# Performance work log

Hardware: AMD Instinct MI355X
Metric: run time of the kernel (lower is better)

Reference implementation:

```python
import jax, jax.numpy as jnp
import numpy as np

N_W, N_E, N_UP, N_DN = 4096, 32, 16, 16
D, N_LAYERS, K_DET = 64, 3, 16
BOX = 6.0


def _ln(x, g, b, eps=1e-5):
    mu = x.mean(-1, keepdims=True)
    v = ((x - mu) ** 2).mean(-1, keepdims=True)
    return (x - mu) / jnp.sqrt(v + eps) * g + b


def setup_inputs() -> dict:
    key = jax.random.key(0)
    ks = jax.random.split(key, 24)
    f32 = jnp.float32

    def w(k, shape, s=0.1):
        return (jax.random.normal(k, shape) * s).astype(f32)

    cell = (BOX * jnp.eye(3)).astype(f32)
    twist = w(ks[0], (3,), 0.3)
    r_electrons = (jax.random.uniform(ks[1], (N_W, N_E, 3)) * BOX).astype(f32)
    inp = dict(
        r_electrons=r_electrons, cell=cell, twist=twist,
        W_e=w(ks[2], (3, D)), b_e=w(ks[3], (D,), 0.05),
        W_pw=w(ks[4], (6, D)), b_pw=w(ks[5], (D,), 0.05),
        W1=w(ks[6], (N_LAYERS, 3 * D, D)), b1=w(ks[7], (N_LAYERS, D), 0.05),
        W2=w(ks[8], (N_LAYERS, D, D)), b2=w(ks[9], (N_LAYERS, D), 0.05),
        ln_w=jnp.ones((N_LAYERS, D), f32), ln_b=jnp.zeros((N_LAYERS, D), f32),
        W_up=w(ks[10], (D, K_DET * N_UP)), b_up=w(ks[11], (K_DET * N_UP,), 0.05),
        W_dn=w(ks[12], (D, K_DET * N_DN)), b_dn=w(ks[13], (K_DET * N_DN,), 0.05),
        det_weights=jnp.zeros((K_DET,), f32),
        Wj1=w(ks[14], (1, 32)), bj1=w(ks[15], (32,), 0.05),
        Wj2=w(ks[16], (32, 32)), bj2=w(ks[17], (32,), 0.05),
        Wj3=w(ks[18], (32, 1)), bj3=w(ks[19], (1,), 0.05),
        jastrow_scale=jnp.asarray(0.1, f32),
    )
    return inp


def reference(r_electrons, cell, twist, W_e, b_e, W_pw, b_pw, W1, b1, W2, b2,
              ln_w, ln_b, W_up, b_up, W_dn, b_dn, det_weights,
              Wj1, bj1, Wj2, bj2, Wj3, bj3, jastrow_scale):
    L_inv = jnp.linalg.inv(cell)
    # wrap to cell via fractional coords
    s = r_electrons @ L_inv.T
    r = (s - jnp.floor(s)) @ cell  # [Nw, Ne, 3]
    # plane-wave features on wrapped positions
    s2 = r @ L_inv.T
    two_pi = 2.0 * jnp.pi
    pw = jnp.concatenate([jnp.sin(two_pi * s2), jnp.cos(two_pi * s2)], axis=-1)
    h = r @ W_e + b_e + pw @ W_pw + b_pw  # [Nw, Ne, D]
    # mean-field interaction layers
    for l in range(W1.shape[0]):
        hm = jnp.broadcast_to(h.mean(axis=1, keepdims=True), h.shape)
        x = jnp.concatenate([h, hm, h * hm], axis=-1)  # [Nw, Ne, 3D]
        delta = jax.nn.silu(x @ W1[l] + b1[l]) @ W2[l] + b2[l]
        h = _ln(h + delta, ln_w[l], ln_b[l])
    # minimum-image pairwise distances
    d = r[:, :, None, :] - r[:, None, :, :]  # [Nw, Ne, Ne, 3]
    sij = d @ L_inv.T
    vec = (sij - jnp.round(sij)) @ cell
    r_ij = jnp.linalg.norm(vec, axis=-1)  # [Nw, Ne, Ne]
    iu, ju = np.triu_indices(r.shape[1], 1)
    rp = r_ij[:, iu, ju][..., None]  # [Nw, P, 1]
    j = jax.nn.silu(rp @ Wj1 + bj1)
    j = jax.nn.silu(j @ Wj2 + bj2)
    j = (j @ Wj3 + bj3)[..., 0]
    jastrow = jastrow_scale * j.sum(axis=1)  # [Nw]
    # multi-determinant combine (vectorized over K via signed logsumexp)
    K = det_weights.shape[0]
    n_up = W_up.shape[1] // K
    n_dn = W_dn.shape[1] // K
    orb_up = h[:, :n_up] @ W_up + b_up  # [Nw, n_up, K*n_up]
    phi_up = jnp.moveaxis(orb_up.reshape(-1, n_up, K, n_up), 2, 1)  # [Nw,K,n_up,n_up]
    su, lu = jnp.linalg.slogdet(phi_up)
    orb_dn = h[:, n_up:] @ W_dn + b_dn
    phi_dn = jnp.moveaxis(orb_dn.reshape(-1, n_dn, K, n_dn), 2, 1)
    sd, ld = jnp.linalg.slogdet(phi_dn)
    logs = lu + ld + jnp.log(jax.nn.softmax(det_weights) + 1e-10)[None, :]  # [Nw,K]
    signs = su * sd
    m = jnp.max(logs, axis=1, keepdims=True)
    ssum = jnp.sum(signs * jnp.exp(logs - m), axis=1)
    log_psi = jastrow + m[:, 0] + jnp.log(jnp.abs(ssum) + 1e-30)
    sign_psi = jnp.sign(ssum)
    return log_psi, sign_psi
```

## Files before the change

kernel.cpp:

```cpp
#include <hip/hip_runtime.h>

#define N_WALK 4096
#define N_EL   32
#define DIM    64
#define HPAD   66
#define NLAY   3
#define KDET   16
#define NPAIR  496
#define TWO_PI_D 6.283185307179586476925286766559
#define JTAB_N    8192
#define JTAB_RMAX 5.25f

using f64x4 = __attribute__((ext_vector_type(4))) double;

#define MFMA64(A, B, C) __builtin_amdgcn_mfma_f64_16x16x4f64((A), (B), (C), 0, 0, 0)

__device__ __forceinline__ double exp_d(double x) {
  const double LOG2E  = 1.4426950408889634074;
  const double LN2_HI = 6.93147180369123816490e-01;
  const double LN2_LO = 1.90821492927058770002e-10;
  const double nf = rint(x * LOG2E);
  double r = fma(-nf, LN2_HI, x);
  r = fma(-nf, LN2_LO, r);
  double p = 1.0/3628800.0;
  p = fma(p, r, 1.0/362880.0);
  p = fma(p, r, 1.0/40320.0);
  p = fma(p, r, 1.0/5040.0);
  p = fma(p, r, 1.0/720.0);
  p = fma(p, r, 1.0/120.0);
  p = fma(p, r, 1.0/24.0);
  p = fma(p, r, 1.0/6.0);
  p = fma(p, r, 0.5);
  p = fma(p, r, 1.0);
  p = fma(p, r, 1.0);
  const long long bits = ((long long)((int)nf + 1023)) << 52;
  return p * __longlong_as_double(bits);
}

__device__ __forceinline__ double silu_d(double x) {
  const double d = 1.0 + exp_d(-x);
  const double q0 = (double)(1.0f / (float)d);
  double q = q0 * (2.0 - d * q0);
  q = q * (2.0 - d * q);
  return x * q;
}
__device__ __forceinline__ float silu_q(float x) { return x / (1.0f + __expf(-x)); }

__device__ __forceinline__ void sincos_2pi(double u, double* s, double* c) {
  const double q = rint(u * 4.0);
  const double z = fma(q, -0.25, u);
  const double th = z * TWO_PI_D;
  const double t2 = th * th;
  double ps = -1.0/39916800.0;
  ps = fma(ps, t2, 1.0/362880.0);
  ps = fma(ps, t2, -1.0/5040.0);
  ps = fma(ps, t2, 1.0/120.0);
  ps = fma(ps, t2, -1.0/6.0);
  ps = fma(ps, t2, 1.0);
  const double sn = th * ps;
  double pc = 1.0/479001600.0;
  pc = fma(pc, t2, -1.0/3628800.0);
  pc = fma(pc, t2, 1.0/40320.0);
  pc = fma(pc, t2, -1.0/720.0);
  pc = fma(pc, t2, 1.0/24.0);
  pc = fma(pc, t2, -0.5);
  pc = fma(pc, t2, 1.0);
  const int k = ((int)q) & 3;
  *s = (k==0) ? sn : ((k==1) ? pc : ((k==2) ? -sn : -pc));
  *c = (k==0) ? pc : ((k==1) ? -sn : ((k==2) ? -pc : sn));
}

__global__ __launch_bounds__(256) void jtab_kernel(
    const float* __restrict__ Wj1, const float* __restrict__ bj1,
    const float* __restrict__ Wj2, const float* __restrict__ bj2,
    const float* __restrict__ Wj3, const float* __restrict__ bj3,
    float* __restrict__ tab)
{
  const int i = blockIdx.x * 256 + threadIdx.x;
  if (i > JTAB_N) return;
  const float r = (float)i * (JTAB_RMAX / (float)JTAB_N);
  float h1[32];
  #pragma unroll
  for (int m=0;m<32;m++) h1[m] = silu_q(fmaf(r, Wj1[m], bj1[m]));
  float o = bj3[0];
  for (int n=0;n<32;n++) {
    float a2 = bj2[n];
    #pragma unroll
    for (int m=0;m<32;m++) a2 = fmaf(h1[m], Wj2[m*32+n], a2);
    o = fmaf(silu_q(a2), Wj3[n], o);
  }
  tab[i] = o;
}

__global__ __launch_bounds__(256) void wf_kernel(
    const float* __restrict__ r_el,
    const float* __restrict__ cell,
    const float* __restrict__ W_e,  const float* __restrict__ b_e,
    const float* __restrict__ W_pw, const float* __restrict__ b_pw,
    const float* __restrict__ W1,   const float* __restrict__ b1,
    const float* __restrict__ W2,   const float* __restrict__ b2,
    const float* __restrict__ ln_w, const float* __restrict__ ln_b,
    const float* __restrict__ W_up, const float* __restrict__ b_up,
    const float* __restrict__ W_dn, const float* __restrict__ b_dn,
    const float* __restrict__ det_w,
    const float* __restrict__ jtab,
    const float* __restrict__ jscale,
    float* __restrict__ out)
{
  __shared__ float s_linv[9];
  __shared__ float s_cl[9];
  __shared__ float s_r[N_EL][3];
  __shared__ float s_h[N_EL][HPAD];
  __shared__ float s_u[16*257];
  __shared__ float s_hm[DIM];
  __shared__ double s_hb[DIM];
  __shared__ double s_lu[2][KDET];
  __shared__ float  s_su[2][KDET];
  __shared__ float  s_red[4];
#define SY(e,d)   s_u[(e)*HPAD + (d)]
#define SPW(e,i)  s_u[2112 + (e)*6 + (i)]
#define SORB(j,c) s_u[(j)*257 + (c)]

  const int t = threadIdx.x;
  const int w = blockIdx.x;
  const int wv = t >> 6;
  const int l  = t & 63;
  const int lr = l & 15;
  const int lq = l >> 4;

  if (t == 0) {
    double m00=cell[0], m01=cell[1], m02=cell[2];
    double m10=cell[3], m11=cell[4], m12=cell[5];
    double m20=cell[6], m21=cell[7], m22=cell[8];
    double c00 = m11*m22 - m12*m21;
    double c10 = m12*m20 - m10*m22;
    double c20 = m10*m21 - m11*m20;
    double det = m00*c00 + m01*c10 + m02*c20;
    double id = 1.0/det;
    s_linv[0]=(float)(c00*id); s_linv[1]=(float)((m02*m21-m01*m22)*id); s_linv[2]=(float)((m01*m12-m02*m11)*id);
    s_linv[3]=(float)(c10*id); s_linv[4]=(float)((m00*m22-m02*m20)*id); s_linv[5]=(float)((m02*m10-m00*m12)*id);
    s_linv[6]=(float)(c20*id); s_linv[7]=(float)((m01*m20-m00*m21)*id); s_linv[8]=(float)((m00*m11-m01*m10)*id);
    #pragma unroll
    for (int i=0;i<9;i++) s_cl[i]=cell[i];
  }
  __syncthreads();

  if (t < 128) {
    const int e = t >> 2, ax = t & 3;
    const float* rp = r_el + ((size_t)w * N_EL + e) * 3;
    const float rx = rp[0], ry = rp[1], rz = rp[2];
    float s0 = (float)((double)s_linv[0]*rx + (double)s_linv[1]*ry + (double)s_linv[2]*rz);
    float s1 = (float)((double)s_linv[3]*rx + (double)s_linv[4]*ry + (double)s_linv[5]*rz);
    float s2 = (float)((double)s_linv[6]*rx + (double)s_linv[7]*ry + (double)s_linv[8]*rz);
    s0 -= floorf(s0); s1 -= floorf(s1); s2 -= floorf(s2);
    const float wx = (float)((double)s0*s_cl[0] + (double)s1*s_cl[3] + (double)s2*s_cl[6]);
    const float wy = (float)((double)s0*s_cl[1] + (double)s1*s_cl[4] + (double)s2*s_cl[7]);
    const float wz = (float)((double)s0*s_cl[2] + (double)s1*s_cl[5] + (double)s2*s_cl[8]);
    if (ax == 3) {
      s_r[e][0]=wx; s_r[e][1]=wy; s_r[e][2]=wz;
    } else {
      const float u = (float)((double)s_linv[3*ax+0]*wx + (double)s_linv[3*ax+1]*wy + (double)s_linv[3*ax+2]*wz);
      double sn, cs;
      sincos_2pi((double)u, &sn, &cs);
      SPW(e, ax)   = (float)sn;
      SPW(e, ax+3) = (float)cs;
    }
  }
  __syncthreads();

  {
    const int e = t >> 3, db = (t & 7) * 8;
    const double rx=s_r[e][0], ry=s_r[e][1], rz=s_r[e][2];
    const double p0=SPW(e,0),p1=SPW(e,1),p2=SPW(e,2);
    const double p3=SPW(e,3),p4=SPW(e,4),p5=SPW(e,5);
    #pragma unroll
    for (int u=0;u<8;u++) {
      const int d = db+u;
      double acc = (double)b_e[d] + (double)b_pw[d];
      acc = fma(rx, (double)W_e[0*DIM+d], acc);
      acc = fma(ry, (double)W_e[1*DIM+d], acc);
      acc = fma(rz, (double)W_e[2*DIM+d], acc);
      acc = fma(p0, (double)W_pw[0*DIM+d], acc);
      acc = fma(p1, (double)W_pw[1*DIM+d], acc);
      acc = fma(p2, (double)W_pw[2*DIM+d], acc);
      acc = fma(p3, (double)W_pw[3*DIM+d], acc);
      acc = fma(p4, (double)W_pw[4*DIM+d], acc);
      acc = fma(p5, (double)W_pw[5*DIM+d], acc);
      s_h[e][d] = (float)acc;
    }
  }
  __syncthreads();

  const int m  = wv & 1;
  const int nb = (wv >> 1) * 2;
  const int ea = m*16 + lr;
  const int c0 = nb*16 + lr;
  const int er = m*16 + lq*4;

  for (int L = 0; L < NLAY; ++L) {
    const float* __restrict__ w1p = W1 + (size_t)L*192*DIM;
    const float* __restrict__ w2p = W2 + (size_t)L*DIM*DIM;

    {
      double s = 0.0;
      #pragma unroll 8
      for (int e=0;e<N_EL;e++) s += (double)s_h[e][l];
      s_hm[l] = (float)(s * (1.0/N_EL));
      const int c = nb*16 + (l & 31);
      const int half = l >> 5;
      double hb = (half == 0) ? (double)b1[L*DIM + c] : 0.0;
      const int k0 = half*32;
      #pragma unroll 8
      for (int km=k0; km<k0+32; km++)
        hb = fma((double)s_hm[km], (double)w1p[(64+km)*DIM + c], hb);
      hb += __shfl_xor(hb, 32, 64);
      if (half == 0) s_hb[c] = hb;
    }

    {
      f64x4 a0 = {0.0,0.0,0.0,0.0}, a1 = {0.0,0.0,0.0,0.0};
      #pragma unroll
      for (int kk=0;kk<16;kk++) {
        const int km = kk*4 + lq;
        const double af = (double)s_h[ea][km];
        const double q0 = (double)w1p[km*DIM + c0];
        const double q1 = (double)w1p[km*DIM + c0 + 16];
        a0 = MFMA64(af, q0, a0);
        a1 = MFMA64(af, q1, a1);
      }
      #pragma unroll
      for (int kk=0;kk<16;kk++) {
        const int km = kk*4 + lq;
        const double af = (double)(s_h[ea][km] * s_hm[km]);
        const double q0 = (double)w1p[(128+km)*DIM + c0];
        const double q1 = (double)w1p[(128+km)*DIM + c0 + 16];
        a0 = MFMA64(af, q0, a0);
        a1 = MFMA64(af, q1, a1);
      }
      #pragma unroll
      for (int v=0;v<4;v++) {
        const float p0 = (float)(a0[v] + s_hb[c0]);
        const float p1 = (float)(a1[v] + s_hb[c0 + 16]);
        SY(er+v, c0)      = (float)silu_d((double)p0);
        SY(er+v, c0 + 16) = (float)silu_d((double)p1);
      }
    }
    __syncthreads();

    {
      f64x4 a0 = {0.0,0.0,0.0,0.0}, a1 = {0.0,0.0,0.0,0.0};
      #pragma unroll
      for (int kk=0;kk<16;kk++) {
        const int km = kk*4 + lq;
        const double af = (double)SY(ea, km);
        const double q0 = (double)w2p[km*DIM + c0];
        const double q1 = (double)w2p[km*DIM + c0 + 16];
        a0 = MFMA64(af, q0, a0);
        a1 = MFMA64(af, q1, a1);
      }
      #pragma unroll
      for (int v=0;v<4;v++) {
        const float d0 = (float)(a0[v] + (double)b2[L*DIM + c0]);
        const float d1 = (float)(a1[v] + (double)b2[L*DIM + c0 + 16]);
        s_h[er+v][c0]      = s_h[er+v][c0]      + d0;
        s_h[er+v][c0 + 16] = s_h[er+v][c0 + 16] + d1;
      }
    }
    __syncthreads();

    {
      const int e = t >> 3, db = (t & 7) * 8;
      float v[8];
      double ps=0.0, pss=0.0;
      #pragma unroll
      for (int u=0;u<8;u++) {
        v[u] = s_h[e][db+u];
        ps += (double)v[u]; pss += (double)v[u]*(double)v[u];
      }
      #pragma unroll
      for (int off=4; off>=1; off>>=1) {
        ps  += __shfl_xor(ps,  off, 8);
        pss += __shfl_xor(pss, off, 8);
      }
      const double mu = ps * (1.0/DIM);
      double var = pss * (1.0/DIM) - mu*mu;
      var = fmax(var, 0.0);
      const double s = var + 1e-5;
      double rstd = (double)rsqrtf((float)s);
      rstd = rstd * (1.5 - 0.5*s*rstd*rstd);
      rstd = rstd * (1.5 - 0.5*s*rstd*rstd);
      #pragma unroll
      for (int u=0;u<8;u++) {
        const int d = db+u;
        s_h[e][d] = (float)(((double)v[u]-mu)*rstd*(double)ln_w[L*DIM+d] + (double)ln_b[L*DIM+d]);
      }
    }
    __syncthreads();
  }

  float jpart = 0.f;
  for (int p = t; p < NPAIR; p += 256) {
    int i = 0, rem = p;
    while (rem >= (N_EL-1) - i) { rem -= (N_EL-1) - i; ++i; }
    const int j = i + 1 + rem;
    const float dx = s_r[i][0]-s_r[j][0];
    const float dy = s_r[i][1]-s_r[j][1];
    const float dz = s_r[i][2]-s_r[j][2];
    float q0 = (float)((double)s_linv[0]*dx + (double)s_linv[1]*dy + (double)s_linv[2]*dz);
    float q1 = (float)((double)s_linv[3]*dx + (double)s_linv[4]*dy + (double)s_linv[5]*dz);
    float q2 = (float)((double)s_linv[6]*dx + (double)s_linv[7]*dy + (double)s_linv[8]*dz);
    q0 -= rintf(q0); q1 -= rintf(q1); q2 -= rintf(q2);
    const float vx = (float)((double)q0*s_cl[0] + (double)q1*s_cl[3] + (double)q2*s_cl[6]);
    const float vy = (float)((double)q0*s_cl[1] + (double)q1*s_cl[4] + (double)q2*s_cl[7]);
    const float vz = (float)((double)q0*s_cl[2] + (double)q1*s_cl[5] + (double)q2*s_cl[8]);
    const float rij = sqrtf(vx*vx + vy*vy + vz*vz);
    const float u = rij * ((float)JTAB_N / JTAB_RMAX);
    int i0 = (int)u;
    i0 = (i0 > JTAB_N-1) ? (JTAB_N-1) : i0;
    const float fr = u - (float)i0;
    const float f0 = jtab[i0], f1 = jtab[i0+1];
    jpart += fmaf(fr, f1 - f0, f0);
  }
  #pragma unroll
  for (int off=32; off>=1; off>>=1) jpart += __shfl_xor(jpart, off, 64);
  if ((t & 63) == 0) s_red[t >> 6] = jpart;

  {
    const int g4 = wv * 4;
    const int g  = t >> 4;
    const int r  = t & 15;
    double a0r[16], a1r[16];

    __builtin_amdgcn_s_setprio(1);
    #pragma unroll 1
    for (int gi=0; gi<4; ++gi) {
      const int cb = (g4 + gi)*16 + lr;
      f64x4 ac = {0.0,0.0,0.0,0.0};
      #pragma unroll
      for (int kk=0;kk<16;kk++) {
        const int km = kk*4 + lq;
        ac = MFMA64((double)s_h[lr][km], (double)W_up[(size_t)km*256 + cb], ac);
      }
      const int row = lq*4;
      #pragma unroll
      for (int v=0;v<4;v++)
        SORB(row+v, cb) = (float)(ac[v] + (double)b_up[cb]);
    }
    __builtin_amdgcn_s_setprio(0);
    #pragma unroll
    for (int j=0;j<16;j++) a0r[j] = (double)SORB(j, t);

    __builtin_amdgcn_s_setprio(1);
    #pragma unroll 1
    for (int gi=0; gi<4; ++gi) {
      const int cb = (g4 + gi)*16 + lr;
      f64x4 ac = {0.0,0.0,0.0,0.0};
      #pragma unroll
      for (int kk=0;kk<16;kk++) {
        const int km = kk*4 + lq;
        ac = MFMA64((double)s_h[16+lr][km], (double)W_dn[(size_t)km*256 + cb], ac);
      }
      const int row = lq*4;
      #pragma unroll
      for (int v=0;v<4;v++)
        SORB(row+v, cb) = (float)(ac[v] + (double)b_dn[cb]);
    }
    __builtin_amdgcn_s_setprio(0);
    #pragma unroll
    for (int j=0;j<16;j++) a1r[j] = (double)SORB(j, t);

    double prod0 = 1.0, prod1 = 1.0;
    int done0 = 0, done1 = 0, step0 = 0, step1 = 0;
    #pragma unroll
    for (int k=0;k<16;k++) {
      float bv0 = done0 ? -1.0f : (float)fabs(a0r[k]); int bi0 = r;
      float bv1 = done1 ? -1.0f : (float)fabs(a1r[k]); int bi1 = r;
      #pragma unroll
      for (int off=8; off>=1; off>>=1) {
        const float ov0 = __shfl_xor(bv0, off, 16); const int oi0 = __shfl_xor(bi0, off, 16);
        const float ov1 = __shfl_xor(bv1, off, 16); const int oi1 = __shfl_xor(bi1, off, 16);
        if (ov0 > bv0 || (ov0 == bv0 && oi0 < bi0)) { bv0 = ov0; bi0 = oi0; }
        if (ov1 > bv1 || (ov1 == bv1 && oi1 < bi1)) { bv1 = ov1; bi1 = oi1; }
      }
      const int p0 = bi0, p1 = bi1;
      const double piv0 = __shfl(a0r[k], p0, 16);
      const double piv1 = __shfl(a1r[k], p1, 16);
      prod0 *= piv0; prod1 *= piv1;
      if (r == p0) { done0 = 1; step0 = k; }
      if (r == p1) { done1 = 1; step1 = k; }
      const double f0 = (!done0 && piv0 != 0.0) ? a0r[k]/piv0 : 0.0;
      const double f1 = (!done1 && piv1 != 0.0) ? a1r[k]/piv1 : 0.0;
      #pragma unroll
      for (int j=k+1;j<16;j++) {
        const double kj0 = __shfl(a0r[j], p0, 16);
        const double kj1 = __shfl(a1r[j], p1, 16);
        a0r[j] = fma(-f0, kj0, a0r[j]);
        a1r[j] = fma(-f1, kj1, a1r[j]);
      }
    }
    int inv0 = 0, inv1 = 0;
    #pragma unroll
    for (int s2=0;s2<16;s2++) {
      const int os0 = __shfl(step0, s2, 16);
      const int os1 = __shfl(step1, s2, 16);
      inv0 += (s2 < r && os0 > step0) ? 1 : 0;
      inv1 += (s2 < r && os1 > step1) ? 1 : 0;
    }
    #pragma unroll
    for (int off=8; off>=1; off>>=1) {
      inv0 += __shfl_xor(inv0, off, 16);
      inv1 += __shfl_xor(inv1, off, 16);
    }
    if (r == 0) {
      s_lu[0][g] = log(fabs(prod0));
      s_su[0][g] = ((inv0 + ((prod0 < 0.0) ? 1 : 0)) & 1) ? -1.f : 1.f;
      s_lu[1][g] = log(fabs(prod1));
      s_su[1][g] = ((inv1 + ((prod1 < 0.0) ? 1 : 0)) & 1) ? -1.f : 1.f;
    }
  }
  __syncthreads();

  if (t < 16) {
    const int k = t;
    const double wwk = (double)det_w[k];
    double mw = wwk;
    #pragma unroll
    for (int off=8; off>=1; off>>=1) mw = fmax(mw, __shfl_xor(mw, off, 16));
    const double ew = exp_d(wwk - mw);
    double sum = ew;
    #pragma unroll
    for (int off=8; off>=1; off>>=1) sum += __shfl_xor(sum, off, 16);
    const double lg = s_lu[0][k] + s_lu[1][k] + log(ew/sum + 1e-10);
    const double sg = (double)(s_su[0][k] * s_su[1][k]);
    double m2 = lg;
    #pragma unroll
    for (int off=8; off>=1; off>>=1) m2 = fmax(m2, __shfl_xor(m2, off, 16));
    double ssum = sg * exp_d(lg - m2);
    #pragma unroll
    for (int off=8; off>=1; off>>=1) ssum += __shfl_xor(ssum, off, 16);
    if (t == 0) {
      const double jas = (double)jscale[0] * (double)(s_red[0]+s_red[1]+s_red[2]+s_red[3]);
      out[w] = (float)(jas + m2 + log(fabs(ssum) + 1e-30));
      out[N_WALK + w] = (ssum > 0.0) ? 1.f : ((ssum < 0.0) ? -1.f : 0.f);
    }
  }
}

extern "C" void kernel_launch(void* const* d_in, const int* in_sizes, int n_in,
                              void* d_out, int out_size, void* d_ws, size_t ws_size,
                              hipStream_t stream) {
  const float* r_el  = (const float*)d_in[0];
  const float* cell  = (const float*)d_in[1];
  const float* W_e   = (const float*)d_in[3];
  const float* b_e   = (const float*)d_in[4];
  const float* W_pw  = (const float*)d_in[5];
  const float* b_pw  = (const float*)d_in[6];
  const float* W1    = (const float*)d_in[7];
  const float* b1    = (const float*)d_in[8];
  const float* W2    = (const float*)d_in[9];
  const float* b2    = (const float*)d_in[10];
  const float* ln_w  = (const float*)d_in[11];
  const float* ln_b  = (const float*)d_in[12];
  const float* W_up  = (const float*)d_in[13];
  const float* b_up  = (const float*)d_in[14];
  const float* W_dn  = (const float*)d_in[15];
  const float* b_dn  = (const float*)d_in[16];
  const float* det_w = (const float*)d_in[17];
  const float* Wj1   = (const float*)d_in[18];
  const float* bj1   = (const float*)d_in[19];
  const float* Wj2   = (const float*)d_in[20];
  const float* bj2   = (const float*)d_in[21];
  const float* Wj3   = (const float*)d_in[22];
  const float* bj3   = (const float*)d_in[23];
  const float* jsc   = (const float*)d_in[24];
  float* jtab = (float*)d_ws;

  jtab_kernel<<<(JTAB_N + 1 + 255) / 256, 256, 0, stream>>>(
      Wj1, bj1, Wj2, bj2, Wj3, bj3, jtab);

  wf_kernel<<<N_WALK, 256, 0, stream>>>(
      r_el, cell, W_e, b_e, W_pw, b_pw, W1, b1, W2, b2, ln_w, ln_b,
      W_up, b_up, W_dn, b_dn, det_w, jtab, jsc,
      (float*)d_out);
}
```

Baseline: 441.7 us.

## Process up/down determinants sequentially with per-wave LDS slabs to cut registers

Restructures the orbital/determinant stage so each wave handles its own four determinants per spin, one spin at a time, staging orbitals in a small per-wave LDS slab instead of a shared 16x257 buffer. This halves the live double-precision matrix registers (one 16-entry array instead of two) and shrinks shared memory, and a launch-bounds hint requests 7 blocks per SM. The intent is higher occupancy; the cost is less ILP from interleaving two eliminations and possible spills if the register cap is too tight.

```diff
diff --git a/kernel.cpp b/kernel.cpp
--- a/kernel.cpp
+++ b/kernel.cpp
@@ -92,7 +92,7 @@
   tab[i] = o;
 }
 
-__global__ __launch_bounds__(256) void wf_kernel(
+__global__ __launch_bounds__(256, 7) void wf_kernel(
     const float* __restrict__ r_el,
     const float* __restrict__ cell,
     const float* __restrict__ W_e,  const float* __restrict__ b_e,
@@ -111,15 +111,15 @@
   __shared__ float s_cl[9];
   __shared__ float s_r[N_EL][3];
   __shared__ float s_h[N_EL][HPAD];
-  __shared__ float s_u[16*257];
+  __shared__ float s_u[2304];
   __shared__ float s_hm[DIM];
   __shared__ double s_hb[DIM];
   __shared__ double s_lu[2][KDET];
   __shared__ float  s_su[2][KDET];
   __shared__ float  s_red[4];
-#define SY(e,d)   s_u[(e)*HPAD + (d)]
-#define SPW(e,i)  s_u[2112 + (e)*6 + (i)]
-#define SORB(j,c) s_u[(j)*257 + (c)]
+#define SY(e,d)    s_u[(e)*HPAD + (d)]
+#define SPW(e,i)   s_u[2112 + (e)*6 + (i)]
+#define SLAB(j,c)  s_u[wv*528 + (j)*33 + (c)]
 
   const int t = threadIdx.x;
   const int w = blockIdx.x;
@@ -327,95 +327,71 @@
 
   {
     const int g4 = wv * 4;
-    const int g  = t >> 4;
-    const int r  = t & 15;
-    double a0r[16], a1r[16];
-
-    __builtin_amdgcn_s_setprio(1);
+    const int g_loc = lq;
+    const int r = lr;
     #pragma unroll 1
-    for (int gi=0; gi<4; ++gi) {
-      const int cb = (g4 + gi)*16 + lr;
-      f64x4 ac = {0.0,0.0,0.0,0.0};
-      #pragma unroll
-      for (int kk=0;kk<16;kk++) {
-        const int km = kk*4 + lq;
-        ac = MFMA64((double)s_h[lr][km], (double)W_up[(size_t)km*256 + cb], ac);
-      }
-      const int row = lq*4;
-      #pragma unroll
-      for (int v=0;v<4;v++)
-        SORB(row+v, cb) = (float)(ac[v] + (double)b_up[cb]);
-    }
-    __builtin_amdgcn_s_setprio(0);
-    #pragma unroll
-    for (int j=0;j<16;j++) a0r[j] = (double)SORB(j, t);
-
-    __builtin_amdgcn_s_setprio(1);
-    #pragma unroll 1
-    for (int gi=0; gi<4; ++gi) {
-      const int cb = (g4 + gi)*16 + lr;
-      f64x4 ac = {0.0,0.0,0.0,0.0};
-      #pragma unroll
-      for (int kk=0;kk<16;kk++) {
-        const int km = kk*4 + lq;
-        ac = MFMA64((double)s_h[16+lr][km], (double)W_dn[(size_t)km*256 + cb], ac);
-      }
-      const int row = lq*4;
-      #pragma unroll
-      for (int v=0;v<4;v++)
-        SORB(row+v, cb) = (float)(ac[v] + (double)b_dn[cb]);
-    }
-    __builtin_amdgcn_s_setprio(0);
-    #pragma unroll
-    for (int j=0;j<16;j++) a1r[j] = (double)SORB(j, t);
-
-    double prod0 = 1.0, prod1 = 1.0;
-    int done0 = 0, done1 = 0, step0 = 0, step1 = 0;
-    #pragma unroll
-    for (int k=0;k<16;k++) {
-      float bv0 = done0 ? -1.0f : (float)fabs(a0r[k]); int bi0 = r;
-      float bv1 = done1 ? -1.0f : (float)fabs(a1r[k]); int bi1 = r;
-      #pragma unroll
-      for (int off=8; off>=1; off>>=1) {
-        const float ov0 = __shfl_xor(bv0, off, 16); const int oi0 = __shfl_xor(bi0, off, 16);
-        const float ov1 = __shfl_xor(bv1, off, 16); const int oi1 = __shfl_xor(bi1, off, 16);
-        if (ov0 > bv0 || (ov0 == bv0 && oi0 < bi0)) { bv0 = ov0; bi0 = oi0; }
-        if (ov1 > bv1 || (ov1 == bv1 && oi1 < bi1)) { bv1 = ov1; bi1 = oi1; }
-      }
-      const int p0 = bi0, p1 = bi1;
-      const double piv0 = __shfl(a0r[k], p0, 16);
-      const double piv1 = __shfl(a1r[k], p1, 16);
-      prod0 *= piv0; prod1 *= piv1;
-      if (r == p0) { done0 = 1; step0 = k; }
-      if (r == p1) { done1 = 1; step1 = k; }
-      const double f0 = (!done0 && piv0 != 0.0) ? a0r[k]/piv0 : 0.0;
-      const double f1 = (!done1 && piv1 != 0.0) ? a1r[k]/piv1 : 0.0;
-      #pragma unroll
-      for (int j=k+1;j<16;j++) {
-        const double kj0 = __shfl(a0r[j], p0, 16);
-        const double kj1 = __shfl(a1r[j], p1, 16);
-        a0r[j] = fma(-f0, kj0, a0r[j]);
-        a1r[j] = fma(-f1, kj1, a1r[j]);
-      }
-    }
-    int inv0 = 0, inv1 = 0;
-    #pragma unroll
-    for (int s2=0;s2<16;s2++) {
-      const int os0 = __shfl(step0, s2, 16);
-      const int os1 = __shfl(step1, s2, 16);
-      inv0 += (s2 < r && os0 > step0) ? 1 : 0;
-      inv1 += (s2 < r && os1 > step1) ? 1 : 0;
-    }
-    #pragma unroll
-    for (int off=8; off>=1; off>>=1) {
-      inv0 += __shfl_xor(inv0, off, 16);
-      inv1 += __shfl_xor(inv1, off, 16);
-    }
-    if (r == 0) {
-      s_lu[0][g] = log(fabs(prod0));
-      s_su[0][g] = ((inv0 + ((prod0 < 0.0) ? 1 : 0)) & 1) ? -1.f : 1.f;
-      s_lu[1][g] = log(fabs(prod1));
-      s_su[1][g] = ((inv1 + ((prod1 < 0.0) ? 1 : 0)) & 1) ? -1.f : 1.f;
+    for (int sp=0; sp<2; ++sp) {
+      const float* __restrict__ Wo = sp ? W_dn : W_up;
+      const float* __restrict__ bo = sp ? b_dn : b_up;
+      const int arow = sp*16 + lr;
+      double a[16];
+      #pragma unroll 1
+      for (int b=0; b<2; ++b) {
+        __builtin_amdgcn_s_setprio(1);
+        #pragma unroll
+        for (int gi=0; gi<2; ++gi) {
+          const int cb = (g4 + 2*b + gi)*16 + lr;
+          f64x4 ac = {0.0,0.0,0.0,0.0};
+          #pragma unroll
+          for (int kk=0;kk<16;kk++) {
+            const int km = kk*4 + lq;
+            ac = MFMA64((double)s_h[arow][km], (double)Wo[(size_t)km*256 + cb], ac);
+          }
+          const int row = lq*4;
+          #pragma unroll
+          for (int v=0;v<4;v++)
+            SLAB(row+v, gi*16 + lr) = (float)(ac[v] + (double)bo[cb]);
+        }
+        __builtin_amdgcn_s_setprio(0);
+        if ((g_loc >> 1) == b) {
+          #pragma unroll
+          for (int j=0;j<16;j++) a[j] = (double)SLAB(j, (g_loc & 1)*16 + r);
+        }
+        __builtin_amdgcn_sched_barrier(0);
+      }
+      double prod = 1.0;
+      int done = 0, step = 0;
+      #pragma unroll
+      for (int k=0;k<16;k++) {
+        float bv = done ? -1.0f : (float)fabs(a[k]); int bi = r;
+        #pragma unroll
+        for (int off=8; off>=1; off>>=1) {
+          const float ov = __shfl_xor(bv, off, 16); const int oi = __shfl_xor(bi, off, 16);
+          if (ov > bv || (ov == bv && oi < bi)) { bv = ov; bi = oi; }
+        }
+        const int p = bi;
+        const double piv = __shfl(a[k], p, 16);
+        prod *= piv;
+        if (r == p) { done = 1; step = k; }
+        const double f = (!done && piv != 0.0) ? a[k]/piv : 0.0;
+        #pragma unroll
+        for (int j=k+1;j<16;j++) {
+          const double kj = __shfl(a[j], p, 16);
+          a[j] = fma(-f, kj, a[j]);
+        }
+      }
+      int inv = 0;
+      #pragma unroll
+      for (int s2=0;s2<16;s2++) {
+        const int os = __shfl(step, s2, 16);
+        inv += (s2 < r && os > step) ? 1 : 0;
+      }
+      #pragma unroll
+      for (int off=8; off>=1; off>>=1) inv += __shfl_xor(inv, off, 16);
+      if (r == 0) {
+        s_lu[sp][g4 + g_loc] = log(fabs(prod));
+        s_su[sp][g4 + g_loc] = ((inv + ((prod < 0.0) ? 1 : 0)) & 1) ? -1.f : 1.f;
+      }
     }
   }
   __syncthreads();
```

Result: slower. 768.4 us (+73.9%).
